# Kernel tuning notes

Hardware: AMD Instinct MI355X
Metric: run time of the kernel (lower is better)

Reference implementation:

```python
import jax, jax.numpy as jnp
import numpy as np

D_MODEL = 768
D_STATE = 128
D_CONV = 4
EXPAND = 4
D_INNER = EXPAND * D_MODEL  # 3072
DT_RANK = 48  # ceil(768/16), mamba default dt_rank='auto'
H_MLP = 768
EPS = 1e-6


def setup_inputs() -> dict:
    key = jax.random.key(0)
    ks = jax.random.split(key, 12)
    B, T = 1, 384

    def rn(k, shape, s=0.02):
        return jax.random.normal(k, shape, jnp.float32) * s

    inp = {}
    inp["x"] = jax.random.normal(ks[0], (B, 3 * T, D_MODEL), jnp.float32)
    inp["ln_w"] = jnp.ones((6, D_MODEL), jnp.float32)  # ln1..ln6 RMSNorm weights
    # 3 independent Mamba blocks, params stacked on leading dim
    inp["in_proj_w"] = rn(ks[1], (3, 2 * D_INNER, D_MODEL))
    inp["conv_w"] = rn(ks[2], (3, D_INNER, 1, D_CONV), 0.1)  # depthwise causal conv1d
    inp["conv_b"] = rn(ks[3], (3, D_INNER), 0.1)
    inp["x_proj_w"] = rn(ks[4], (3, DT_RANK + 2 * D_STATE, D_INNER))
    inp["dt_proj_w"] = rn(ks[5], (3, D_INNER, DT_RANK), 0.1)
    inp["dt_proj_b"] = rn(ks[6], (3, D_INNER), 0.1) - 4.0  # small dt after softplus
    A = jnp.tile(jnp.arange(1, D_STATE + 1, dtype=jnp.float32)[None, None, :], (3, D_INNER, 1))
    inp["A_log"] = jnp.log(A)  # mamba S4D-real init
    inp["D_skip"] = jnp.ones((3, D_INNER), jnp.float32)
    inp["out_proj_w"] = rn(ks[7], (3, D_MODEL, D_INNER))
    # 3 GatedMLPs: fc1 -> 2*hidden (value, gate), silu gate, fc2 -> out
    inp["fc1_w"] = rn(ks[8], (3, 2 * H_MLP, D_MODEL))
    inp["fc1_b"] = jnp.zeros((3, 2 * H_MLP), jnp.float32)
    inp["fc2_w"] = rn(ks[9], (3, D_MODEL, H_MLP))
    inp["fc2_b"] = jnp.zeros((3, D_MODEL), jnp.float32)
    return inp


def _rmsnorm(x, w):
    v = jnp.mean(jnp.square(x), axis=-1, keepdims=True)
    return x * jax.lax.rsqrt(v + EPS) * w


def _mamba(u, in_w, cw, cb, xp_w, dt_w, dt_b, A_log, D_skip, out_w):
    # u: (B, T, D_MODEL)
    Bsz = u.shape[0]
    xz = u @ in_w.T  # (B,T,2*Di)
    x, z = jnp.split(xz, 2, axis=-1)
    # causal depthwise conv1d over time
    xc = jax.lax.conv_general_dilated(
        jnp.swapaxes(x, 1, 2), cw, (1,), [(D_CONV - 1, 0)],
        feature_group_count=D_INNER)  # (B,Di,T)
    x = jax.nn.silu(jnp.swapaxes(xc, 1, 2) + cb)  # (B,T,Di)
    x_dbl = x @ xp_w.T  # (B,T,dt_rank+2N)
    dt = x_dbl[..., :DT_RANK]
    Bm = x_dbl[..., DT_RANK:DT_RANK + D_STATE]
    Cm = x_dbl[..., DT_RANK + D_STATE:]
    delta = jax.nn.softplus(dt @ dt_w.T + dt_b)  # (B,T,Di)
    A = -jnp.exp(A_log)  # (Di,N)

    def step(h, inp):
        d_t, B_t, C_t, u_t = inp  # (B,Di),(B,N),(B,N),(B,Di)
        h = jnp.exp(d_t[:, :, None] * A) * h + (d_t * u_t)[:, :, None] * B_t[:, None, :]
        y = jnp.einsum('bdn,bn->bd', h, C_t)
        return h, y

    h0 = jnp.zeros((Bsz, D_INNER, D_STATE), u.dtype)
    xs = tuple(jnp.swapaxes(a, 0, 1) for a in (delta, Bm, Cm, x))  # time-major
    _, ys = jax.lax.scan(jax.checkpoint(step), h0, xs)
    y = jnp.swapaxes(ys, 0, 1) + x * D_skip  # (B,T,Di)
    return (y * jax.nn.silu(z)) @ out_w.T  # (B,T,D_MODEL)


def _gmlp(x, w1, b1, w2, b2):
    h = x @ w1.T + b1
    a, g = jnp.split(h, 2, axis=-1)
    return (jax.nn.silu(g) * a) @ w2.T + b2


def reference(x, ln_w, in_proj_w, conv_w, conv_b, x_proj_w, dt_proj_w, dt_proj_b,
              A_log, D_skip, out_proj_w, fc1_w, fc1_b, fc2_w, fc2_b):
    t = x.shape[1] // 3
    outs = []
    for i in range(3):  # music / up / down branches
        b = x[:, i * t:(i + 1) * t]
        b = b + _mamba(_rmsnorm(b, ln_w[2 * i]), in_proj_w[i], conv_w[i], conv_b[i],
                       x_proj_w[i], dt_proj_w[i], dt_proj_b[i], A_log[i], D_skip[i],
                       out_proj_w[i])
        b = b + _gmlp(_rmsnorm(b, ln_w[2 * i + 1]), fc1_w[i], fc1_b[i], fc2_w[i], fc2_b[i])
        outs.append(b)
    return jnp.concatenate(outs, axis=1)
```

## Files before the change

kernel.cpp:

```cpp
#include <hip/hip_runtime.h>
#include <hip/hip_bf16.h>

#define TSEQ 384
#define DMODEL 768
#define DINNER 3072
#define DSTATE 128
#define DTRANK 48
#define XPROJ_N (DTRANK + 2*DSTATE)
#define NSEG 3
#define LOG2E 1.44269504088896340736f
#define LN2F  0.69314718055994530942f

typedef __attribute__((ext_vector_type(8))) short short8;
typedef __attribute__((ext_vector_type(4))) float floatx4;
typedef unsigned short u16;
typedef unsigned int u32;

__device__ __forceinline__ float bf2f(u16 u) {
    return __uint_as_float(((unsigned)u) << 16);
}
__device__ __forceinline__ float ldf(const void* p, size_t i, int bf) {
    return bf ? bf2f(((const u16*)p)[i]) : ((const float*)p)[i];
}
__device__ __forceinline__ void stf(void* p, size_t i, float v, int bf) {
    if (bf) ((__hip_bfloat16*)p)[i] = __float2bfloat16(v);
    else    ((float*)p)[i] = v;
}
__device__ __forceinline__ float silu_f(float v) { return v / (1.f + __expf(-v)); }
__device__ __forceinline__ u16 f2bf(float f) {
    unsigned u = __float_as_uint(f);
    return (u16)((u + 0x7FFFu + ((u >> 16) & 1u)) >> 16);
}

__device__ __forceinline__ float exp2_fast(float x) {
#if __has_builtin(__builtin_amdgcn_exp2f)
    return __builtin_amdgcn_exp2f(x);
#else
    return exp2f(x);
#endif
}

template<int CTRL>
__device__ __forceinline__ float ror_add(float x) {
    int r = __builtin_amdgcn_update_dpp(0, __float_as_int(x), CTRL, 0xF, 0xF, true);
    return x + __int_as_float(r);
}

__device__ __forceinline__ void gl16(const void* g, void* l) {
    __builtin_amdgcn_global_load_lds(
        (const __attribute__((address_space(1))) u32*)g,
        (__attribute__((address_space(3))) u32*)l, 16, 0, 0);
}

__global__ void k_detect(const unsigned* lnw_bits, int* flag) {
    if (threadIdx.x == 0) {
        flag[0] = (lnw_bits[0] == 0x3F803F80u) ? 1 : 0;
    }
}

__global__ __launch_bounds__(256) void k_rmsnorm(
    const void* src, int src_is_f32, const void* lnw, int wbase,
    u16* out, const int* flagp)
{
    int bf  = *flagp;
    int sbf = src_is_f32 ? 0 : bf;
    int r   = blockIdx.x;
    int seg = r / TSEQ;
    int wrow = 2*seg + wbase;
    int tid = threadIdx.x;
    float v[3]; float s = 0.f;
    #pragma unroll
    for (int j = 0; j < 3; ++j) {
        int e = j*256 + tid;
        v[j] = ldf(src, (size_t)r*DMODEL + e, sbf);
        s += v[j]*v[j];
    }
    __shared__ float red[256];
    red[tid] = s; __syncthreads();
    for (int st = 128; st > 0; st >>= 1) {
        if (tid < st) red[tid] += red[tid+st];
        __syncthreads();
    }
    float rs = rsqrtf(red[0]/(float)DMODEL + 1e-6f);
    #pragma unroll
    for (int j = 0; j < 3; ++j) {
        int e = j*256 + tid;
        out[(size_t)r*DMODEL + e] = f2bf(v[j]*rs*ldf(lnw, (size_t)wrow*DMODEL + e, bf));
    }
}

__global__ __launch_bounds__(256) void k_gemm(
    const float* A, const void* W, const void* bias,
    float* C, const int* flagp, int M, int N, int K, int lda)
{
    int bf  = *flagp;
    int seg = blockIdx.z;
    int mbase = blockIdx.y * 64, nbase = blockIdx.x * 64;
    int tid = threadIdx.x;
    int tx = tid & 15, ty = tid >> 4;

    __shared__ float As[16][68];
    __shared__ float Ws[16][68];

    const float* Ag = A + (size_t)seg*M*lda;
    size_t segW = (size_t)seg*N*K;

    int lrow = tid >> 2;
    int lk   = (tid & 3) * 4;
    int wn   = nbase + lrow;

    float acc[4][4];
    #pragma unroll
    for (int i = 0; i < 4; ++i)
        #pragma unroll
        for (int j = 0; j < 4; ++j) acc[i][j] = 0.f;

    for (int kt = 0; kt < K; kt += 16) {
        float4 av = *reinterpret_cast<const float4*>(Ag + (size_t)(mbase+lrow)*lda + kt + lk);
        As[lk+0][lrow] = av.x; As[lk+1][lrow] = av.y;
        As[lk+2][lrow] = av.z; As[lk+3][lrow] = av.w;
        float w0=0.f, w1=0.f, w2=0.f, w3=0.f;
        if (wn < N) {
            size_t off = segW + (size_t)wn*K + kt + lk;
            if (bf) {
                ushort4 q = *reinterpret_cast<const ushort4*>((const u16*)W + off);
                w0 = bf2f(q.x); w1 = bf2f(q.y); w2 = bf2f(q.z); w3 = bf2f(q.w);
            } else {
                float4 f = *reinterpret_cast<const float4*>((const float*)W + off);
                w0 = f.x; w1 = f.y; w2 = f.z; w3 = f.w;
            }
        }
        Ws[lk+0][lrow] = w0; Ws[lk+1][lrow] = w1;
        Ws[lk+2][lrow] = w2; Ws[lk+3][lrow] = w3;
        __syncthreads();
        #pragma unroll
        for (int kk = 0; kk < 16; ++kk) {
            float4 a4 = *reinterpret_cast<const float4*>(&As[kk][ty*4]);
            float4 b4 = *reinterpret_cast<const float4*>(&Ws[kk][tx*4]);
            float ar[4] = {a4.x, a4.y, a4.z, a4.w};
            float br[4] = {b4.x, b4.y, b4.z, b4.w};
            #pragma unroll
            for (int i = 0; i < 4; ++i)
                #pragma unroll
                for (int j = 0; j < 4; ++j)
                    acc[i][j] = fmaf(ar[i], br[j], acc[i][j]);
        }
        __syncthreads();
    }

    #pragma unroll
    for (int i = 0; i < 4; ++i) {
        int m = mbase + ty*4 + i;
        #pragma unroll
        for (int j = 0; j < 4; ++j) {
            int n = nbase + tx*4 + j;
            if (n < N) {
                float v = acc[i][j] + ldf(bias, (size_t)seg*N + n, bf);
                v = (v > 20.f) ? v : log1pf(__expf(v));
                C[((size_t)(seg*M + m))*N + n] = v;
            }
        }
    }
}

#define LPITCH 40
__global__ __launch_bounds__(256) void k_gemm_mfma128(
    const u16* A, const void* W, u16* C, const int* flagp,
    int M, int N, int K)
{
    int bf  = *flagp;
    int seg = blockIdx.z;
    int mbase = blockIdx.y * 128, nbase = blockIdx.x * 128;
    int tid = threadIdx.x;
    int w = tid >> 6, lane = tid & 63;
    int wm = w >> 1, wn = w & 1;
    int quad = lane >> 4, l16 = lane & 15;

    __shared__ short As[128 * LPITCH];
    __shared__ short Ws[128 * LPITCH];

    const u16* Ag = A + (size_t)seg*M*K + (size_t)mbase*K;
    size_t segW = (size_t)seg*N*K;

    int sr  = tid >> 1;
    int skc = (tid & 1) * 16;

    floatx4 acc[4][4];
    #pragma unroll
    for (int i = 0; i < 4; ++i)
        #pragma unroll
        for (int j = 0; j < 4; ++j)
            acc[i][j] = (floatx4){0.f, 0.f, 0.f, 0.f};

    int wrow = nbase + sr;
    for (int kt = 0; kt < K; kt += 32) {
        const u16* ap = Ag + (size_t)sr*K + kt + skc;
        *reinterpret_cast<short8*>(&As[sr*LPITCH + skc])     = *reinterpret_cast<const short8*>(ap);
        *reinterpret_cast<short8*>(&As[sr*LPITCH + skc + 8]) = *reinterpret_cast<const short8*>(ap + 8);
        {
            short8 s0 = (short8){0,0,0,0,0,0,0,0}, s1 = s0;
            if (wrow < N) {
                size_t off = segW + (size_t)wrow*K + kt + skc;
                if (bf) {
                    s0 = *reinterpret_cast<const short8*>((const u16*)W + off);
                    s1 = *reinterpret_cast<const short8*>((const u16*)W + off + 8);
                } else {
                    const float* wp = (const float*)W + off;
                    float f[16];
                    #pragma unroll
                    for (int q = 0; q < 4; ++q) {
                        float4 v = *reinterpret_cast<const float4*>(wp + q*4);
                        f[q*4+0] = v.x; f[q*4+1] = v.y; f[q*4+2] = v.z; f[q*4+3] = v.w;
                    }
                    #pragma unroll
                    for (int q = 0; q < 8; ++q) { s0[q] = (short)f2bf(f[q]); s1[q] = (short)f2bf(f[q+8]); }
                }
            }
            *reinterpret_cast<short8*>(&Ws[sr*LPITCH + skc])     = s0;
            *reinterpret_cast<short8*>(&Ws[sr*LPITCH + skc + 8]) = s1;
        }
        __syncthreads();
        short8 af[4], bfr[4];
        #pragma unroll
        for (int i = 0; i < 4; ++i)
            af[i] = *reinterpret_cast<const short8*>(&As[(wm*64 + i*16 + l16)*LPITCH + quad*8]);
        #pragma unroll
        for (int j = 0; j < 4; ++j)
            bfr[j] = *reinterpret_cast<const short8*>(&Ws[(wn*64 + j*16 + l16)*LPITCH + quad*8]);
        #pragma unroll
        for (int i = 0; i < 4; ++i)
            #pragma unroll
            for (int j = 0; j < 4; ++j)
                acc[i][j] = __builtin_amdgcn_mfma_f32_16x16x32_bf16(af[i], bfr[j], acc[i][j], 0, 0, 0);
        __syncthreads();
    }

    #pragma unroll
    for (int i = 0; i < 4; ++i) {
        #pragma unroll
        for (int reg = 0; reg < 4; ++reg) {
            int grow = mbase + wm*64 + i*16 + quad*4 + reg;
            #pragma unroll
            for (int j = 0; j < 4; ++j) {
                int gcol = nbase + wn*64 + j*16 + l16;
                if (gcol < N)
                    C[((size_t)(seg*M + grow))*N + gcol] = f2bf(acc[i][j][reg]);
            }
        }
    }
}

#define LP2 72
__global__ __launch_bounds__(256) void k_gemm_mfma64(
    const u16* A, const void* W, const void* bias, const void* resid,
    int resid_flagged, void* C, int c_mode, const int* flagp,
    int M, int N, int K)
{
    int bf  = *flagp;
    int seg = blockIdx.z;
    int mbase = blockIdx.y * 64, nbase = blockIdx.x * 64;
    int tid = threadIdx.x;
    int w = tid >> 6, lane = tid & 63;
    int wm = w >> 1, wn = w & 1;
    int quad = lane >> 4, l16 = lane & 15;

    __shared__ short As[64 * LP2];
    __shared__ short Ws[64 * LP2];

    const u16* Ag = A + (size_t)seg*M*K + (size_t)mbase*K;
    size_t segW = (size_t)seg*N*K;

    int sr  = tid >> 2;
    int skc = (tid & 3) * 16;

    floatx4 acc[2][2];
    #pragma unroll
    for (int i = 0; i < 2; ++i)
        #pragma unroll
        for (int j = 0; j < 2; ++j)
            acc[i][j] = (floatx4){0.f, 0.f, 0.f, 0.f};

    int wrow = nbase + sr;
    for (int kt = 0; kt < K; kt += 64) {
        const u16* ap = Ag + (size_t)sr*K + kt + skc;
        *reinterpret_cast<short8*>(&As[sr*LP2 + skc])     = *reinterpret_cast<const short8*>(ap);
        *reinterpret_cast<short8*>(&As[sr*LP2 + skc + 8]) = *reinterpret_cast<const short8*>(ap + 8);
        {
            short8 s0 = (short8){0,0,0,0,0,0,0,0}, s1 = s0;
            if (wrow < N) {
                size_t off = segW + (size_t)wrow*K + kt + skc;
                if (bf) {
                    s0 = *reinterpret_cast<const short8*>((const u16*)W + off);
                    s1 = *reinterpret_cast<const short8*>((const u16*)W + off + 8);
                } else {
                    const float* wp = (const float*)W + off;
                    float f[16];
                    #pragma unroll
                    for (int q = 0; q < 4; ++q) {
                        float4 v = *reinterpret_cast<const float4*>(wp + q*4);
                        f[q*4+0] = v.x; f[q*4+1] = v.y; f[q*4+2] = v.z; f[q*4+3] = v.w;
                    }
                    #pragma unroll
                    for (int q = 0; q < 8; ++q) { s0[q] = (short)f2bf(f[q]); s1[q] = (short)f2bf(f[q+8]); }
                }
            }
            *reinterpret_cast<short8*>(&Ws[sr*LP2 + skc])     = s0;
            *reinterpret_cast<short8*>(&Ws[sr*LP2 + skc + 8]) = s1;
        }
        __syncthreads();
        #pragma unroll
        for (int kk = 0; kk < 2; ++kk) {
            short8 af[2], bfr[2];
            #pragma unroll
            for (int i = 0; i < 2; ++i)
                af[i] = *reinterpret_cast<const short8*>(&As[(wm*32 + i*16 + l16)*LP2 + kk*32 + quad*8]);
            #pragma unroll
            for (int j = 0; j < 2; ++j)
                bfr[j] = *reinterpret_cast<const short8*>(&Ws[(wn*32 + j*16 + l16)*LP2 + kk*32 + quad*8]);
            #pragma unroll
            for (int i = 0; i < 2; ++i)
                #pragma unroll
                for (int j = 0; j < 2; ++j)
                    acc[i][j] = __builtin_amdgcn_mfma_f32_16x16x32_bf16(af[i], bfr[j], acc[i][j], 0, 0, 0);
        }
        __syncthreads();
    }

    #pragma unroll
    for (int i = 0; i < 2; ++i) {
        #pragma unroll
        for (int reg = 0; reg < 4; ++reg) {
            int grow = mbase + wm*32 + i*16 + quad*4 + reg;
            #pragma unroll
            for (int j = 0; j < 2; ++j) {
                int gcol = nbase + wn*32 + j*16 + l16;
                if (gcol < N) {
                    float v = acc[i][j][reg];
                    if (bias) v += ldf(bias, (size_t)seg*N + gcol, bf);
                    size_t idx = ((size_t)(seg*M + grow))*N + gcol;
                    if (resid) v += resid_flagged ? ldf(resid, idx, bf)
                                                  : ((const float*)resid)[idx];
                    if      (c_mode == 0) ((float*)C)[idx] = v;
                    else if (c_mode == 1) ((u16*)C)[idx] = f2bf(v);
                    else                  stf(C, idx, v, bf);
                }
            }
        }
    }
}

__global__ __launch_bounds__(256) void k_fc1_gate(
    const u16* A, const void* W, const void* bias, u16* act, const int* flagp)
{
    const int M = TSEQ, K = DMODEL, NF = 2*DMODEL;
    int bf  = *flagp;
    int seg = blockIdx.z;
    int mbase = blockIdx.y * 64, nbase = blockIdx.x * 64;
    int tid = threadIdx.x;
    int w = tid >> 6, lane = tid & 63;
    int wm = w >> 1, wn = w & 1;
    int quad = lane >> 4, l16 = lane & 15;

    __shared__ short As[64 * LPITCH];
    __shared__ short Wa[64 * LPITCH];
    __shared__ short Wg[64 * LPITCH];

    const u16* Ag = A + (size_t)seg*M*K + (size_t)mbase*K;
    size_t segW = (size_t)seg*NF*K;

    int sr  = tid >> 2;
    int skc = (tid & 3) * 8;

    floatx4 acca[2][2], accg[2][2];
    #pragma unroll
    for (int i = 0; i < 2; ++i)
        #pragma unroll
        for (int j = 0; j < 2; ++j) {
            acca[i][j] = (floatx4){0.f, 0.f, 0.f, 0.f};
            accg[i][j] = (floatx4){0.f, 0.f, 0.f, 0.f};
        }

    int wra = nbase + sr;
    int wrg = nbase + DMODEL + sr;
    for (int kt = 0; kt < K; kt += 32) {
        *reinterpret_cast<short8*>(&As[sr*LPITCH + skc]) =
            *reinterpret_cast<const short8*>(Ag + (size_t)sr*K + kt + skc);
        #pragma unroll
        for (int half = 0; half < 2; ++half) {
            int wrow = half ? wrg : wra;
            short* dst = half ? Wg : Wa;
            short8 s;
            size_t off = segW + (size_t)wrow*K + kt + skc;
            if (bf) {
                s = *reinterpret_cast<const short8*>((const u16*)W + off);
            } else {
                const float* wp = (const float*)W + off;
                float4 v0 = *reinterpret_cast<const float4*>(wp);
                float4 v1 = *reinterpret_cast<const float4*>(wp + 4);
                s[0]=(short)f2bf(v0.x); s[1]=(short)f2bf(v0.y); s[2]=(short)f2bf(v0.z); s[3]=(short)f2bf(v0.w);
                s[4]=(short)f2bf(v1.x); s[5]=(short)f2bf(v1.y); s[6]=(short)f2bf(v1.z); s[7]=(short)f2bf(v1.w);
            }
            *reinterpret_cast<short8*>(&dst[sr*LPITCH + skc]) = s;
        }
        __syncthreads();
        short8 af[2], ba[2], bg[2];
        #pragma unroll
        for (int i = 0; i < 2; ++i)
            af[i] = *reinterpret_cast<const short8*>(&As[(wm*32 + i*16 + l16)*LPITCH + quad*8]);
        #pragma unroll
        for (int j = 0; j < 2; ++j) {
            ba[j] = *reinterpret_cast<const short8*>(&Wa[(wn*32 + j*16 + l16)*LPITCH + quad*8]);
            bg[j] = *reinterpret_cast<const short8*>(&Wg[(wn*32 + j*16 + l16)*LPITCH + quad*8]);
        }
        #pragma unroll
        for (int i = 0; i < 2; ++i)
            #pragma unroll
            for (int j = 0; j < 2; ++j) {
                acca[i][j] = __builtin_amdgcn_mfma_f32_16x16x32_bf16(af[i], ba[j], acca[i][j], 0, 0, 0);
                accg[i][j] = __builtin_amdgcn_mfma_f32_16x16x32_bf16(af[i], bg[j], accg[i][j], 0, 0, 0);
            }
        __syncthreads();
    }

    #pragma unroll
    for (int i = 0; i < 2; ++i) {
        #pragma unroll
        for (int reg = 0; reg < 4; ++reg) {
            int grow = mbase + wm*32 + i*16 + quad*4 + reg;
            #pragma unroll
            for (int j = 0; j < 2; ++j) {
                int gcol = nbase + wn*32 + j*16 + l16;
                float va = acca[i][j][reg] + ldf(bias, (size_t)seg*NF + gcol, bf);
                float vg = accg[i][j][reg] + ldf(bias, (size_t)seg*NF + DMODEL + gcol, bf);
                act[((size_t)(seg*M + grow))*DMODEL + gcol] = f2bf(va * silu_f(vg));
            }
        }
    }
}

__global__ __launch_bounds__(256) void k_conv(
    const u16* xz, const void* cw, const void* cb, u16* xconv, const int* flagp)
{
    int bf = *flagp;
    size_t gid = (size_t)blockIdx.x*256 + threadIdx.x;
    int d = (int)(gid % DINNER);
    size_t rt = gid / DINNER;
    int t = (int)(rt % TSEQ);
    int seg = (int)(rt / TSEQ);
    float acc = ldf(cb, (size_t)seg*DINNER + d, bf);
    const u16* xs = xz + (size_t)seg*TSEQ*(2*DINNER);
    #pragma unroll
    for (int j = 0; j < 4; ++j) {
        int ts = t - 3 + j;
        if (ts >= 0)
            acc = fmaf(ldf(cw, ((size_t)seg*DINNER + d)*4 + j, bf),
                       bf2f(xs[(size_t)ts*(2*DINNER) + d]), acc);
    }
    xconv[gid] = f2bf(silu_f(acc));
}

#define WSCH 4
#define WSCT 8
#define NTILE (TSEQ/WSCT)

__global__ __launch_bounds__(64, 4) void k_scan_wave(
    const float* delta, const u16* xconv, const float* xdbl, const u16* xz,
    const void* A_log, const void* D_skip, u16* yout, const int* flagp)
{
    int bf   = flagp[0];
    int seg  = blockIdx.y;
    int dbase = blockIdx.x * WSCH;
    int lane = threadIdx.x;
    int ch = lane >> 4, sl = lane & 15;
    int d = dbase + ch;

    __shared__ float4 BUF[2][WSCT][64];
    __shared__ float  DLB[WSCT][WSCH];
    __shared__ u16    UB[WSCT][WSCH];

    float a[8];
    size_t abase = ((size_t)seg*DINNER + d)*DSTATE + (size_t)sl*8;
    #pragma unroll
    for (int j = 0; j < 8; ++j)
        a[j] = -__expf(ldf(A_log, abase + j, bf)) * LOG2E;
    float gl[8]; float gmax = 0.f;
    gl[0] = 0.f;
    #pragma unroll
    for (int j = 1; j < 8; ++j) {
        gl[j] = (a[j] - a[j-1]) * LN2F;
        gmax = fmaxf(gmax, fabsf(gl[j]));
    }
    float a0  = a[0];
    float Dsk = ldf(D_skip, (size_t)seg*DINNER + d, bf);

    const float* xdbl_s = xdbl + (size_t)seg*TSEQ*XPROJ_N;
    int loff = DTRANK + (lane & 15)*8 + ((lane >> 4) & 1)*4 + ((lane >> 5) ? DSTATE : 0);
    const float* srcl = xdbl_s + loff;

    const float* delta_s = delta + (size_t)seg*TSEQ*DINNER + dbase;
    const u16*   xconv_s = xconv + (size_t)seg*TSEQ*DINNER + dbase;
    const u16*   z_s     = xz    + (size_t)seg*TSEQ*(2*DINNER) + DINNER + dbase + ch;
    u16*         y_s     = yout  + (size_t)seg*TSEQ*DINNER + dbase + ch;

    float4  pdel;
    ushort4 pu;

    auto STAGE = [&](int tile, int buf) {
        const float* rb = srcl + (size_t)tile*WSCT*XPROJ_N;
        #pragma unroll
        for (int t = 0; t < WSCT; ++t)
            gl16(rb + (size_t)t*XPROJ_N, &BUF[buf][t][0]);
    };
    auto PLOAD = [&](int tile) {
        if (lane < WSCT) {
            size_t ro = (size_t)(tile*WSCT + lane)*DINNER;
            pdel = *reinterpret_cast<const float4*>(delta_s + ro);
            pu   = *reinterpret_cast<const ushort4*>(xconv_s + ro);
        }
    };

    float h[8];
    #pragma unroll
    for (int j = 0; j < 8; ++j) h[j] = 0.f;
    float yr = 0.f;

    STAGE(0, 0);
    PLOAD(0);

    int cur = 0;
    for (int tile = 0; tile < NTILE; ++tile) {
        asm volatile("s_waitcnt vmcnt(0)" ::: "memory");
        if (lane < WSCT) {
            *reinterpret_cast<float4*>(&DLB[lane][0]) = pdel;
            *reinterpret_cast<ushort4*>(&UB[lane][0]) = pu;
        }
        if (tile + 1 < NTILE) {
            STAGE(tile + 1, cur ^ 1);
            PLOAD(tile + 1);
        }
        __builtin_amdgcn_sched_barrier(0);

        int half8 = (tile & 1) << 3;
        #pragma unroll
        for (int t = 0; t < WSCT; ++t) {
            float del = DLB[t][ch];
            float ut  = bf2f(UB[t][ch]);
            float du  = del * ut;
            const float4* bp = &BUF[cur][t][0];
            float4 b0 = bp[sl];
            float4 b1 = bp[16 + sl];
            float4 c0 = bp[32 + sl];
            float4 c1 = bp[48 + sl];
            float e0, e1, e2, e3, e4, e5, e6, e7;
            if (__any(del * gmax > 0.04f)) {
                e0 = exp2_fast(del*a[0]); e1 = exp2_fast(del*a[1]);
                e2 = exp2_fast(del*a[2]); e3 = exp2_fast(del*a[3]);
                e4 = exp2_fast(del*a[4]); e5 = exp2_fast(del*a[5]);
                e6 = exp2_fast(del*a[6]); e7 = exp2_fast(del*a[7]);
            } else {
                e0 = exp2_fast(del * a0);
                e1 = e0 * fmaf(del, gl[1], 1.f);
                e2 = e1 * fmaf(del, gl[2], 1.f);
                e3 = e2 * fmaf(del, gl[3], 1.f);
                e4 = e3 * fmaf(del, gl[4], 1.f);
                e5 = e4 * fmaf(del, gl[5], 1.f);
                e6 = e5 * fmaf(del, gl[6], 1.f);
                e7 = e6 * fmaf(del, gl[7], 1.f);
            }
            h[0] = fmaf(e0, h[0], du*b0.x);
            h[1] = fmaf(e1, h[1], du*b0.y);
            h[2] = fmaf(e2, h[2], du*b0.z);
            h[3] = fmaf(e3, h[3], du*b0.w);
            h[4] = fmaf(e4, h[4], du*b1.x);
            h[5] = fmaf(e5, h[5], du*b1.y);
            h[6] = fmaf(e6, h[6], du*b1.z);
            h[7] = fmaf(e7, h[7], du*b1.w);
            float p0 = (sl == 0) ? ut*Dsk : 0.f;
            p0 = fmaf(h[0], c0.x, p0);
            p0 = fmaf(h[1], c0.y, p0);
            p0 = fmaf(h[2], c0.z, p0);
            p0 = fmaf(h[3], c0.w, p0);
            float p1 = h[4]*c1.x;
            p1 = fmaf(h[5], c1.y, p1);
            p1 = fmaf(h[6], c1.z, p1);
            p1 = fmaf(h[7], c1.w, p1);
            float p = p0 + p1;
            p = ror_add<0x128>(p);
            p = ror_add<0x124>(p);
            p = ror_add<0x122>(p);
            p = ror_add<0x121>(p);
            if (sl == (half8 | t)) yr = p;
        }
        if (tile & 1) {
            size_t trow = (size_t)((tile - 1) * WSCT + sl);
            float z = bf2f(z_s[trow * (size_t)(2*DINNER)]);
            y_s[trow * (size_t)DINNER] = f2bf(yr * silu_f(z));
            yr = 0.f;
        }
        cur ^= 1;
    }
}

extern "C" void kernel_launch(void* const* d_in, const int* in_sizes, int n_in,
                              void* d_out, int out_size, void* d_ws, size_t ws_size,
                              hipStream_t stream) {
    const void* x     = d_in[0];
    const void* lnw   = d_in[1];
    const void* inw   = d_in[2];
    const void* convw = d_in[3];
    const void* convb = d_in[4];
    const void* xpw   = d_in[5];
    const void* dtw   = d_in[6];
    const void* dtb   = d_in[7];
    const void* alog  = d_in[8];
    const void* dsk   = d_in[9];
    const void* outw  = d_in[10];
    const void* fc1w  = d_in[11];
    const void* fc1b  = d_in[12];
    const void* fc2w  = d_in[13];
    const void* fc2b  = d_in[14];

    int* flag = (int*)d_ws;
    char* wsb = (char*)d_ws;
    const size_t N_U    = (size_t)NSEG*TSEQ*DMODEL;
    const size_t N_XZ   = (size_t)NSEG*TSEQ*2*DINNER;
    const size_t N_XC   = (size_t)NSEG*TSEQ*DINNER;
    const size_t N_XDBL = (size_t)NSEG*TSEQ*XPROJ_N;

    u16*   u     = (u16*)(wsb + 16);
    u16*   xz    = u + N_U;
    u16*   xconv = xz + N_XZ;
    float* xdbl  = (float*)(xconv + N_XC);
    float* delta = xdbl + N_XDBL;
    u16*   yfin  = (u16*)(delta + N_XC);
    float* b1    = (float*)(yfin + N_XC);
    u16*   actb  = (u16*)(b1 + N_U);

    k_detect<<<1, 64, 0, stream>>>((const unsigned*)lnw, flag);

    k_rmsnorm<<<NSEG*TSEQ, 256, 0, stream>>>(x, 0, lnw, 0, u, flag);
    k_gemm_mfma128<<<dim3(48, 3, NSEG), 256, 0, stream>>>(u, inw,
        xz, flag, TSEQ, 2*DINNER, DMODEL);
    k_conv<<<(NSEG*TSEQ*DINNER)/256, 256, 0, stream>>>(xz, convw, convb, xconv, flag);
    k_gemm_mfma64<<<dim3(5, 6, NSEG), 256, 0, stream>>>(xconv, xpw, nullptr, nullptr, 0,
        xdbl, 0, flag, TSEQ, XPROJ_N, DINNER);
    k_gemm<<<dim3(48, 6, NSEG), 256, 0, stream>>>(xdbl, dtw, dtb,
        delta, flag, TSEQ, DINNER, DTRANK, XPROJ_N);

    k_scan_wave<<<dim3(DINNER/WSCH, NSEG), 64, 0, stream>>>(
        delta, xconv, xdbl, xz, alog, dsk, yfin, flag);

    k_gemm_mfma64<<<dim3(12, 6, NSEG), 256, 0, stream>>>(yfin, outw, nullptr, x, 1,
        b1, 0, flag, TSEQ, DMODEL, DINNER);

    k_rmsnorm<<<NSEG*TSEQ, 256, 0, stream>>>(b1, 1, lnw, 1, u, flag);
    k_fc1_gate<<<dim3(12, 6, NSEG), 256, 0, stream>>>(u, fc1w, fc1b, actb, flag);
    k_gemm_mfma64<<<dim3(12, 6, NSEG), 256, 0, stream>>>(actb, fc2w, fc2b, b1, 0,
        d_out, 2, flag, TSEQ, DMODEL, DMODEL);
}
```

Measured before the change: 592.4 us.

## Batch scan reductions with transpose-style swizzle and hoist per-tile exp guard

The selective scan now processes tile pairs. It buffers the 16 per-timestep partial dot products and reduces them together with a recursive-halving swizzle, so each lane ends up holding one timestep's result. This replaces four DPP row-rotate adds per timestep. The fast-versus-exact exp guard is now decided once per 8-step tile from the tile's max delta and a wave-wide gmax, instead of a vote every timestep. Delta and u are packed into one LDS array and the z load is prefetched early. The cost is more registers (q[16]) and a slightly more conservative guard.

```diff
diff --git a/kernel.cpp b/kernel.cpp
--- a/kernel.cpp
+++ b/kernel.cpp
@@ -40,9 +40,9 @@
 #endif
 }
 
-template<int CTRL>
-__device__ __forceinline__ float ror_add(float x) {
-    int r = __builtin_amdgcn_update_dpp(0, __float_as_int(x), CTRL, 0xF, 0xF, true);
+template<int MASK>
+__device__ __forceinline__ float swz_add(float x) {
+    int r = __builtin_amdgcn_ds_swizzle(__float_as_int(x), MASK);
     return x + __int_as_float(r);
 }
 
@@ -461,7 +461,8 @@
 
 #define WSCH 4
 #define WSCT 8
-#define NTILE (TSEQ/WSCT)
+#define NPAIR (TSEQ/(2*WSCT))
+#define GUARD_TH 0.04f
 
 __global__ __launch_bounds__(64, 4) void k_scan_wave(
     const float* delta, const u16* xconv, const float* xdbl, const u16* xz,
@@ -475,8 +476,7 @@
     int d = dbase + ch;
 
     __shared__ float4 BUF[2][WSCT][64];
-    __shared__ float  DLB[WSCT][WSCH];
-    __shared__ u16    UB[WSCT][WSCH];
+    __shared__ float  DLB2[WSCT][8];
 
     float a[8];
     size_t abase = ((size_t)seg*DINNER + d)*DSTATE + (size_t)sl*8;
@@ -490,8 +490,12 @@
         gl[j] = (a[j] - a[j-1]) * LN2F;
         gmax = fmaxf(gmax, fabsf(gl[j]));
     }
+    float wg = gmax;
+    #pragma unroll
+    for (int k = 32; k >= 1; k >>= 1) wg = fmaxf(wg, __shfl_xor(wg, k));
     float a0  = a[0];
     float Dsk = ldf(D_skip, (size_t)seg*DINNER + d, bf);
+    float dskg = (sl == 0) ? Dsk : 0.f;
 
     const float* xdbl_s = xdbl + (size_t)seg*TSEQ*XPROJ_N;
     int loff = DTRANK + (lane & 15)*8 + ((lane >> 4) & 1)*4 + ((lane >> 5) ? DSTATE : 0);
@@ -502,8 +506,9 @@
     const u16*   z_s     = xz    + (size_t)seg*TSEQ*(2*DINNER) + DINNER + dbase + ch;
     u16*         y_s     = yout  + (size_t)seg*TSEQ*DINNER + dbase + ch;
 
-    float4  pdel;
-    ushort4 pu;
+    float4  pdel = (float4){0.f, 0.f, 0.f, 0.f};
+    ushort4 pu   = (ushort4){0, 0, 0, 0};
+    u16     pz   = 0;
 
     auto STAGE = [&](int tile, int buf) {
         const float* rb = srcl + (size_t)tile*WSCT*XPROJ_N;
@@ -518,87 +523,123 @@
             pu   = *reinterpret_cast<const ushort4*>(xconv_s + ro);
         }
     };
+    auto DSTORE = [&]() -> bool {
+        if (lane < WSCT) {
+            float4 w0 = (float4){pdel.x, bf2f(pu.x), pdel.y, bf2f(pu.y)};
+            float4 w1 = (float4){pdel.z, bf2f(pu.z), pdel.w, bf2f(pu.w)};
+            *reinterpret_cast<float4*>(&DLB2[lane][0]) = w0;
+            *reinterpret_cast<float4*>(&DLB2[lane][4]) = w1;
+        }
+        float m4 = fmaxf(fmaxf(pdel.x, pdel.y), fmaxf(pdel.z, pdel.w));
+        return __any(m4 * wg > GUARD_TH);
+    };
 
     float h[8];
     #pragma unroll
     for (int j = 0; j < 8; ++j) h[j] = 0.f;
-    float yr = 0.f;
+    float q[16];
+
+#define SCAN_STEP(T, K, BI, FAST) do {                                        \
+    float2 du2 = *reinterpret_cast<const float2*>(&DLB2[T][ch*2]);            \
+    float del = du2.x, ut = du2.y;                                            \
+    float du  = del * ut;                                                     \
+    const float4* bp_ = &BUF[BI][T][0];                                       \
+    float4 b0 = bp_[sl];      float4 b1 = bp_[16 + sl];                       \
+    float4 c0 = bp_[32 + sl]; float4 c1 = bp_[48 + sl];                       \
+    float e0,e1,e2,e3,e4,e5,e6,e7;                                            \
+    if (FAST) {                                                               \
+        e0 = exp2_fast(del * a0);                                             \
+        e1 = e0 * fmaf(del, gl[1], 1.f);                                      \
+        e2 = e1 * fmaf(del, gl[2], 1.f);                                      \
+        e3 = e2 * fmaf(del, gl[3], 1.f);                                      \
+        e4 = e3 * fmaf(del, gl[4], 1.f);                                      \
+        e5 = e4 * fmaf(del, gl[5], 1.f);                                      \
+        e6 = e5 * fmaf(del, gl[6], 1.f);                                      \
+        e7 = e6 * fmaf(del, gl[7], 1.f);                                      \
+    } else {                                                                  \
+        e0 = exp2_fast(del*a[0]); e1 = exp2_fast(del*a[1]);                   \
+        e2 = exp2_fast(del*a[2]); e3 = exp2_fast(del*a[3]);                   \
+        e4 = exp2_fast(del*a[4]); e5 = exp2_fast(del*a[5]);                   \
+        e6 = exp2_fast(del*a[6]); e7 = exp2_fast(del*a[7]);                   \
+    }                                                                         \
+    h[0] = fmaf(e0, h[0], du*b0.x);                                           \
+    h[1] = fmaf(e1, h[1], du*b0.y);                                           \
+    h[2] = fmaf(e2, h[2], du*b0.z);                                           \
+    h[3] = fmaf(e3, h[3], du*b0.w);                                           \
+    h[4] = fmaf(e4, h[4], du*b1.x);                                           \
+    h[5] = fmaf(e5, h[5], du*b1.y);                                           \
+    h[6] = fmaf(e6, h[6], du*b1.z);                                           \
+    h[7] = fmaf(e7, h[7], du*b1.w);                                           \
+    float p0 = ut * dskg;                                                     \
+    p0 = fmaf(h[0], c0.x, p0);                                                \
+    p0 = fmaf(h[1], c0.y, p0);                                                \
+    p0 = fmaf(h[2], c0.z, p0);                                                \
+    p0 = fmaf(h[3], c0.w, p0);                                                \
+    float p1 = h[4]*c1.x;                                                     \
+    p1 = fmaf(h[5], c1.y, p1);                                                \
+    p1 = fmaf(h[6], c1.z, p1);                                                \
+    p1 = fmaf(h[7], c1.w, p1);                                                \
+    q[K] = p0 + p1;                                                           \
+} while (0)
 
     STAGE(0, 0);
     PLOAD(0);
 
-    int cur = 0;
-    for (int tile = 0; tile < NTILE; ++tile) {
+    for (int p = 0; p < NPAIR; ++p) {
+        int tA = 2*p;
         asm volatile("s_waitcnt vmcnt(0)" ::: "memory");
-        if (lane < WSCT) {
-            *reinterpret_cast<float4*>(&DLB[lane][0]) = pdel;
-            *reinterpret_cast<ushort4*>(&UB[lane][0]) = pu;
-        }
-        if (tile + 1 < NTILE) {
-            STAGE(tile + 1, cur ^ 1);
-            PLOAD(tile + 1);
-        }
+        bool gA = DSTORE();
+        STAGE(tA + 1, 1);
+        PLOAD(tA + 1);
+        pz = z_s[(size_t)(p*16 + sl) * (size_t)(2*DINNER)];
         __builtin_amdgcn_sched_barrier(0);
-
-        int half8 = (tile & 1) << 3;
-        #pragma unroll
-        for (int t = 0; t < WSCT; ++t) {
-            float del = DLB[t][ch];
-            float ut  = bf2f(UB[t][ch]);
-            float du  = del * ut;
-            const float4* bp = &BUF[cur][t][0];
-            float4 b0 = bp[sl];
-            float4 b1 = bp[16 + sl];
-            float4 c0 = bp[32 + sl];
-            float4 c1 = bp[48 + sl];
-            float e0, e1, e2, e3, e4, e5, e6, e7;
-            if (__any(del * gmax > 0.04f)) {
-                e0 = exp2_fast(del*a[0]); e1 = exp2_fast(del*a[1]);
-                e2 = exp2_fast(del*a[2]); e3 = exp2_fast(del*a[3]);
-                e4 = exp2_fast(del*a[4]); e5 = exp2_fast(del*a[5]);
-                e6 = exp2_fast(del*a[6]); e7 = exp2_fast(del*a[7]);
-            } else {
-                e0 = exp2_fast(del * a0);
-                e1 = e0 * fmaf(del, gl[1], 1.f);
-                e2 = e1 * fmaf(del, gl[2], 1.f);
-                e3 = e2 * fmaf(del, gl[3], 1.f);
-                e4 = e3 * fmaf(del, gl[4], 1.f);
-                e5 = e4 * fmaf(del, gl[5], 1.f);
-                e6 = e5 * fmaf(del, gl[6], 1.f);
-                e7 = e6 * fmaf(del, gl[7], 1.f);
-            }
-            h[0] = fmaf(e0, h[0], du*b0.x);
-            h[1] = fmaf(e1, h[1], du*b0.y);
-            h[2] = fmaf(e2, h[2], du*b0.z);
-            h[3] = fmaf(e3, h[3], du*b0.w);
-            h[4] = fmaf(e4, h[4], du*b1.x);
-            h[5] = fmaf(e5, h[5], du*b1.y);
-            h[6] = fmaf(e6, h[6], du*b1.z);
-            h[7] = fmaf(e7, h[7], du*b1.w);
-            float p0 = (sl == 0) ? ut*Dsk : 0.f;
-            p0 = fmaf(h[0], c0.x, p0);
-            p0 = fmaf(h[1], c0.y, p0);
-            p0 = fmaf(h[2], c0.z, p0);
-            p0 = fmaf(h[3], c0.w, p0);
-            float p1 = h[4]*c1.x;
-            p1 = fmaf(h[5], c1.y, p1);
-            p1 = fmaf(h[6], c1.z, p1);
-            p1 = fmaf(h[7], c1.w, p1);
-            float p = p0 + p1;
-            p = ror_add<0x128>(p);
-            p = ror_add<0x124>(p);
-            p = ror_add<0x122>(p);
-            p = ror_add<0x121>(p);
-            if (sl == (half8 | t)) yr = p;
-        }
-        if (tile & 1) {
-            size_t trow = (size_t)((tile - 1) * WSCT + sl);
-            float z = bf2f(z_s[trow * (size_t)(2*DINNER)]);
-            y_s[trow * (size_t)DINNER] = f2bf(yr * silu_f(z));
-            yr = 0.f;
-        }
-        cur ^= 1;
-    }
+        if (!gA) {
+            #pragma unroll
+            for (int t = 0; t < WSCT; ++t) SCAN_STEP(t, t, 0, 1);
+        } else {
+            #pragma unroll
+            for (int t = 0; t < WSCT; ++t) SCAN_STEP(t, t, 0, 0);
+        }
+        asm volatile("s_waitcnt vmcnt(0)" ::: "memory");
+        bool gB = DSTORE();
+        if (tA + 2 < 2*NPAIR) {
+            STAGE(tA + 2, 0);
+            PLOAD(tA + 2);
+        }
+        __builtin_amdgcn_sched_barrier(0);
+        if (!gB) {
+            #pragma unroll
+            for (int t = 0; t < WSCT; ++t) SCAN_STEP(t, t + 8, 1, 1);
+        } else {
+            #pragma unroll
+            for (int t = 0; t < WSCT; ++t) SCAN_STEP(t, t + 8, 1, 0);
+        }
+        {
+            float s0[16];
+            #pragma unroll
+            for (int i = 0; i < 16; ++i) s0[i] = swz_add<0x201F>(q[i]);
+            float t0[8];
+            #pragma unroll
+            for (int i = 0; i < 8; ++i) t0[i] = (sl & 8) ? s0[i+8] : s0[i];
+            float s1[8];
+            #pragma unroll
+            for (int i = 0; i < 8; ++i) s1[i] = swz_add<0x101F>(t0[i]);
+            float t1[4];
+            #pragma unroll
+            for (int i = 0; i < 4; ++i) t1[i] = (sl & 4) ? s1[i+4] : s1[i];
+            float s2[4];
+            #pragma unroll
+            for (int i = 0; i < 4; ++i) s2[i] = swz_add<0x081F>(t1[i]);
+            float t2[2];
+            #pragma unroll
+            for (int i = 0; i < 2; ++i) t2[i] = (sl & 2) ? s2[i+2] : s2[i];
+            float s3a = swz_add<0x041F>(t2[0]);
+            float s3b = swz_add<0x041F>(t2[1]);
+            float yv = (sl & 1) ? s3b : s3a;
+            y_s[(size_t)(p*16 + sl) * (size_t)DINNER] = f2bf(yv * silu_f(bf2f(pz)));
+        }
+    }
+#undef SCAN_STEP
 }
 
 extern "C" void kernel_launch(void* const* d_in, const int* in_sizes, int n_in,
```

Result: slower. 675.6 us (+14.0%).
